# Performance work log

Hardware: AMD Instinct MI355X
Metric: run time of the kernel (lower is better)

The kernel has to match this reference:

```python
import jax, jax.numpy as jnp
import numpy as np

DIM = 512
HEADS = 8
DIM_HEAD = 64
LANDMARKS = 256
PINV_ITERS = 6
RES_K = 33


def layernorm(x, g, b, eps=1e-5):
    mu = jnp.mean(x, -1, keepdims=True)
    var = jnp.mean((x - mu) ** 2, -1, keepdims=True)
    return (x - mu) / jnp.sqrt(var + eps) * g + b


def moore_penrose_pinv(x, iters=PINV_ITERS):
    abs_x = jnp.abs(x)
    col = abs_x.sum(-1)
    row = abs_x.sum(-2)
    z = jnp.swapaxes(x, -1, -2) / (jnp.max(col) * jnp.max(row))
    I = jnp.eye(x.shape[-1], dtype=x.dtype)
    for _ in range(iters):
        xz = x @ z
        z = 0.25 * z @ (13.0 * I - xz @ (15.0 * I - xz @ (7.0 * I - xz)))
    return z


def nystrom_attention(x, Wqkv, Wout, bout, res_w):
    b, n, _ = x.shape
    m = LANDMARKS
    pad = (m - n % m) % m
    if pad:
        x = jnp.pad(x, ((0, 0), (pad, 0), (0, 0)))  # front pad, as in lucidrains impl
    qkv = x @ Wqkv  # (b, np, 3*inner)
    q, k, v = jnp.split(qkv, 3, axis=-1)
    to_heads = lambda t: t.reshape(b, -1, HEADS, DIM_HEAD).transpose(0, 2, 1, 3)
    q, k, v = to_heads(q), to_heads(k), to_heads(v)  # (b,h,np,d)
    q = q * (DIM_HEAD ** -0.5)
    l = -(-n // m)  # ceil(n/m), tokens per landmark
    ql = q.reshape(b, HEADS, m, l, DIM_HEAD).sum(3) / l  # (b,h,m,d)
    kl = k.reshape(b, HEADS, m, l, DIM_HEAD).sum(3) / l
    sim1 = jnp.einsum('bhid,bhjd->bhij', q, kl)   # (b,h,np,m)
    sim2 = jnp.einsum('bhid,bhjd->bhij', ql, kl)  # (b,h,m,m)
    sim3 = jnp.einsum('bhid,bhjd->bhij', ql, k)   # (b,h,m,np)
    a1 = jax.nn.softmax(sim1, -1)
    a2 = jax.nn.softmax(sim2, -1)
    a3 = jax.nn.softmax(sim3, -1)
    a2_inv = moore_penrose_pinv(a2)
    out = (a1 @ a2_inv) @ (a3 @ v)  # (b,h,np,d)
    # depthwise residual conv along sequence (kernel 33x1, groups=heads, no bias)
    res = jax.lax.conv_general_dilated(
        v, res_w, (1, 1), [(RES_K // 2, RES_K // 2), (0, 0)],
        dimension_numbers=('NCHW', 'OIHW', 'NCHW'), feature_group_count=HEADS)
    out = out + res
    out = out.transpose(0, 2, 1, 3).reshape(b, -1, HEADS * DIM_HEAD)
    out = out @ Wout + bout
    return out[:, -n:]


def depthwise2d(x, w, b, pad):
    y = jax.lax.conv_general_dilated(
        x, w, (1, 1), [(pad, pad), (pad, pad)],
        dimension_numbers=('NCHW', 'OIHW', 'NCHW'), feature_group_count=DIM)
    return y + b[None, :, None, None]


def ppeg(x, H, W, w7, b7, w5, b5, w3, b3):
    B, _, C = x.shape
    cls_tok, feat = x[:, :1], x[:, 1:]
    cnn = feat.transpose(0, 2, 1).reshape(B, C, H, W)
    y = depthwise2d(cnn, w7, b7, 3) + cnn + depthwise2d(cnn, w5, b5, 2) + depthwise2d(cnn, w3, b3, 1)
    y = y.reshape(B, C, H * W).transpose(0, 2, 1)
    return jnp.concatenate([cls_tok, y], axis=1)


def setup_inputs() -> dict:
    key = jax.random.key(0)
    ks = jax.random.split(key, 20)
    s = 0.02
    n_classes = 5
    inp = {
        'data': jax.random.normal(ks[0], (1, 15000, 1024), jnp.float32),
        'W_fc1': jax.random.normal(ks[1], (1024, DIM), jnp.float32) * s,
        'b_fc1': jnp.zeros((DIM,), jnp.float32),
        'cls_token': jax.random.normal(ks[2], (1, 1, DIM), jnp.float32),
        'ln1_g': jnp.ones((DIM,), jnp.float32), 'ln1_b': jnp.zeros((DIM,), jnp.float32),
        'qkv1': jax.random.normal(ks[3], (DIM, 3 * HEADS * DIM_HEAD), jnp.float32) * s,
        'out1_w': jax.random.normal(ks[4], (HEADS * DIM_HEAD, DIM), jnp.float32) * s,
        'out1_b': jnp.zeros((DIM,), jnp.float32),
        'res1': jax.random.normal(ks[5], (HEADS, 1, RES_K, 1), jnp.float32) * s,
        'w7': jax.random.normal(ks[6], (DIM, 1, 7, 7), jnp.float32) * s,
        'b7': jnp.zeros((DIM,), jnp.float32),
        'w5': jax.random.normal(ks[7], (DIM, 1, 5, 5), jnp.float32) * s,
        'b5': jnp.zeros((DIM,), jnp.float32),
        'w3': jax.random.normal(ks[8], (DIM, 1, 3, 3), jnp.float32) * s,
        'b3': jnp.zeros((DIM,), jnp.float32),
        'ln2_g': jnp.ones((DIM,), jnp.float32), 'ln2_b': jnp.zeros((DIM,), jnp.float32),
        'qkv2': jax.random.normal(ks[9], (DIM, 3 * HEADS * DIM_HEAD), jnp.float32) * s,
        'out2_w': jax.random.normal(ks[10], (HEADS * DIM_HEAD, DIM), jnp.float32) * s,
        'out2_b': jnp.zeros((DIM,), jnp.float32),
        'res2': jax.random.normal(ks[11], (HEADS, 1, RES_K, 1), jnp.float32) * s,
        'norm_g': jnp.ones((DIM,), jnp.float32), 'norm_b': jnp.zeros((DIM,), jnp.float32),
        'W_fc2': jax.random.normal(ks[12], (DIM, n_classes), jnp.float32) * s,
        'b_fc2': jnp.zeros((n_classes,), jnp.float32),
    }
    return inp


def reference(data, W_fc1, b_fc1, cls_token, ln1_g, ln1_b, qkv1, out1_w, out1_b, res1,
              w7, b7, w5, b5, w3, b3, ln2_g, ln2_b, qkv2, out2_w, out2_b, res2,
              norm_g, norm_b, W_fc2, b_fc2):
    h = jax.nn.relu(data @ W_fc1 + b_fc1)  # (B, N, 512)
    N = h.shape[1]
    _H = int(np.ceil(np.sqrt(N)))
    _W = _H
    add = _H * _W - N
    h = jnp.concatenate([h, h[:, :add]], axis=1)  # pad to square grid
    B = h.shape[0]
    h = jnp.concatenate([jnp.broadcast_to(cls_token, (B, 1, DIM)), h], axis=1)
    h = h + nystrom_attention(layernorm(h, ln1_g, ln1_b), qkv1, out1_w, out1_b, res1)
    h = ppeg(h, _H, _W, w7, b7, w5, b5, w3, b3)
    h = h + nystrom_attention(layernorm(h, ln2_g, ln2_b), qkv2, out2_w, out2_b, res2)
    h = layernorm(h, norm_g, norm_b)[:, 0]
    logits = h @ W_fc2 + b_fc2
    Y_prob = jax.nn.softmax(logits, -1)
    Y_hat = jnp.argmax(logits, -1)
    return logits, Y_prob, Y_hat
```

## Files before the change

### kernel.cpp

```cpp
#include <hip/hip_runtime.h>
#include <math.h>

#define NP 15360
#define NPQ 15488
#define NTOK 15130
#define HG 123

typedef __attribute__((ext_vector_type(8))) short s8b;
typedef __attribute__((ext_vector_type(4))) float f4;

__device__ inline float bf2f(ushort u) { return __uint_as_float(((unsigned)u) << 16); }
__device__ inline ushort f2bf(float f) {
    unsigned u = __float_as_uint(f);
    unsigned r = (u + 0x7fffu + ((u >> 16) & 1u)) >> 16;
    return (ushort)r;
}

__global__ __launch_bounds__(256)
void gemm_f32(const float* __restrict__ A, int lda, long sA,
              const float* __restrict__ B, int ldb, long sB,
              float* __restrict__ C, int ldc, long sC,
              int M, int N, int K,
              const float* __restrict__ bias,
              const float* __restrict__ E, int ldE, long sE, float eS,
              float cS, int relu, int accum)
{
    A += (long)blockIdx.z * sA;
    B += (long)blockIdx.z * sB;
    C += (long)blockIdx.z * sC;
    if (E) E += (long)blockIdx.z * sE;
    const int m0 = blockIdx.y * 64, n0 = blockIdx.x * 64;
    const int t = threadIdx.x;
    const int tx = t & 15, ty = t >> 4;
    __shared__ float As[16][64];
    __shared__ float Bs[16][64];
    float acc[4][4] = {};
    const int arow = t >> 2, akc = (t & 3) * 4;
    const int brow = t >> 4, bnc = (t & 15) * 4;
    for (int k0 = 0; k0 < K; k0 += 16) {
        float4 av = make_float4(0.f, 0.f, 0.f, 0.f);
        if (m0 + arow < M) av = *(const float4*)(A + (long)(m0 + arow) * lda + k0 + akc);
        As[akc + 0][arow] = av.x; As[akc + 1][arow] = av.y;
        As[akc + 2][arow] = av.z; As[akc + 3][arow] = av.w;
        float4 bv = *(const float4*)(B + (long)(k0 + brow) * ldb + n0 + bnc);
        *(float4*)&Bs[brow][bnc] = bv;
        __syncthreads();
#pragma unroll
        for (int kk = 0; kk < 16; ++kk) {
            float4 a4 = *(const float4*)&As[kk][ty * 4];
            float4 b4 = *(const float4*)&Bs[kk][tx * 4];
            float a[4] = {a4.x, a4.y, a4.z, a4.w};
            float b[4] = {b4.x, b4.y, b4.z, b4.w};
#pragma unroll
            for (int i = 0; i < 4; i++)
#pragma unroll
                for (int j = 0; j < 4; j++) acc[i][j] = fmaf(a[i], b[j], acc[i][j]);
        }
        __syncthreads();
    }
#pragma unroll
    for (int i = 0; i < 4; i++) {
        int m = m0 + ty * 4 + i;
        if (m < M) {
#pragma unroll
            for (int j = 0; j < 4; j++) {
                int n = n0 + tx * 4 + j;
                float v = cS * acc[i][j];
                if (E) v = fmaf(eS, E[(long)m * ldE + n], v);
                if (bias) v += bias[n];
                if (relu) v = fmaxf(v, 0.f);
                if (accum) C[(long)m * ldc + n] += v;
                else C[(long)m * ldc + n] = v;
            }
        }
    }
}

template<int MT, int NT, int WROWS, int WCOLS>
__global__ __launch_bounds__(256)
void gemm_mfma(const ushort* __restrict__ A, int lda, long sA,
               const ushort* __restrict__ Bt, int ldb, long sB,
               float* __restrict__ C, int ldc, long sC,
               int M, int K,
               const float* __restrict__ bias, int relu, int accum)
{
    constexpr int TM = MT * 16 * WROWS;
    constexpr int TN = NT * 16 * WCOLS;
    constexpr int BKP = 40;
    constexpr int AIT = TM / 64;
    constexpr int BIT = TN / 64;
    __shared__ ushort As[TM * BKP];
    __shared__ ushort Bs[TN * BKP];
    A  += (long)blockIdx.z * sA;
    Bt += (long)blockIdx.z * sB;
    C  += (long)blockIdx.z * sC;
    const int t = threadIdx.x;
    const int nwg = gridDim.x * gridDim.y;
    const int flat = blockIdx.y * gridDim.x + blockIdx.x;
    const int q8 = nwg >> 3, r8 = nwg & 7;
    const int xcd = flat & 7, idx = flat >> 3;
    const int swz = (xcd < r8) ? (xcd * (q8 + 1) + idx)
                               : (r8 * (q8 + 1) + (xcd - r8) * q8 + idx);
    const int m0 = (swz / gridDim.x) * TM;
    const int n0 = (swz % gridDim.x) * TN;
    const int w = t >> 6, l = t & 63;
    const int wm = (w / WCOLS) * (MT * 16), wn = (w % WCOLS) * (NT * 16);
    const int lr = l & 15;
    const int lk = (l >> 4) * 8;
    const int srow = t >> 2, skc = (t & 3) * 8;
    f4 acc[MT][NT] = {};
    s8b pa[AIT], pb[BIT];
#pragma unroll
    for (int i = 0; i < AIT; i++)
        pa[i] = *(const s8b*)(A + (long)(m0 + srow + i * 64) * lda + skc);
#pragma unroll
    for (int i = 0; i < BIT; i++)
        pb[i] = *(const s8b*)(Bt + (long)(n0 + srow + i * 64) * ldb + skc);
    for (int k0 = 0; k0 < K; k0 += 32) {
        __syncthreads();
#pragma unroll
        for (int i = 0; i < AIT; i++)
            *(s8b*)(&As[(srow + i * 64) * BKP + skc]) = pa[i];
#pragma unroll
        for (int i = 0; i < BIT; i++)
            *(s8b*)(&Bs[(srow + i * 64) * BKP + skc]) = pb[i];
        if (k0 + 32 < K) {
#pragma unroll
            for (int i = 0; i < AIT; i++)
                pa[i] = *(const s8b*)(A + (long)(m0 + srow + i * 64) * lda + k0 + 32 + skc);
#pragma unroll
            for (int i = 0; i < BIT; i++)
                pb[i] = *(const s8b*)(Bt + (long)(n0 + srow + i * 64) * ldb + k0 + 32 + skc);
        }
        __syncthreads();
        s8b af[MT], bf[NT];
#pragma unroll
        for (int i = 0; i < MT; i++) af[i] = *(const s8b*)(&As[(wm + i * 16 + lr) * BKP + lk]);
#pragma unroll
        for (int j = 0; j < NT; j++) bf[j] = *(const s8b*)(&Bs[(wn + j * 16 + lr) * BKP + lk]);
#pragma unroll
        for (int i = 0; i < MT; i++)
#pragma unroll
            for (int j = 0; j < NT; j++)
                acc[i][j] = __builtin_amdgcn_mfma_f32_16x16x32_bf16(af[i], bf[j], acc[i][j], 0, 0, 0);
    }
    const int orow = (l >> 4) * 4;
#pragma unroll
    for (int i = 0; i < MT; i++) {
#pragma unroll
        for (int r = 0; r < 4; r++) {
            int m = m0 + wm + i * 16 + orow + r;
            if (m < M) {
#pragma unroll
                for (int j = 0; j < NT; j++) {
                    int n = n0 + wn + j * 16 + lr;
                    float vv = acc[i][j][r];
                    if (bias) vv += bias[n];
                    if (relu) vv = fmaxf(vv, 0.f);
                    if (accum) C[(long)m * ldc + n] += vv;
                    else C[(long)m * ldc + n] = vv;
                }
            }
        }
    }
}

__global__ __launch_bounds__(256)
void gemm_nn16(const ushort* __restrict__ A, const ushort* __restrict__ B,
               const ushort* __restrict__ E, ushort* __restrict__ C,
               int N, int K, float cS, float eS, long sAB)
{
    __shared__ ushort As[64 * 40];
    __shared__ ushort Bs[64 * 40];
    A += (long)blockIdx.z * sAB;
    B += (long)blockIdx.z * sAB;
    if (E) E += (long)blockIdx.z * sAB;
    C += (long)blockIdx.z * sAB;
    const int t = threadIdx.x;
    const int m0 = blockIdx.y * 64, n0 = blockIdx.x * 64;
    const int w = t >> 6, l = t & 63;
    const int wm = (w >> 1) * 32, wn = (w & 1) * 32;
    const int lr = l & 15, lk = (l >> 4) * 8;
    f4 acc[2][2] = {};
    for (int k0 = 0; k0 < K; k0 += 32) {
        {
            int row = t >> 2, kc = (t & 3) * 8;
            s8b v = *(const s8b*)(A + (long)(m0 + row) * K + k0 + kc);
            *(s8b*)(&As[row * 40 + kc]) = v;
            int kk = t >> 3, nc = (t & 7) * 8;
            s8b vb = *(const s8b*)(B + (long)(k0 + kk) * N + n0 + nc);
#pragma unroll
            for (int j = 0; j < 8; j++) Bs[(nc + j) * 40 + kk] = ((ushort*)&vb)[j];
        }
        __syncthreads();
        s8b af[2], bf[2];
#pragma unroll
        for (int i = 0; i < 2; i++) af[i] = *(const s8b*)(&As[(wm + i * 16 + lr) * 40 + lk]);
#pragma unroll
        for (int j = 0; j < 2; j++) bf[j] = *(const s8b*)(&Bs[(wn + j * 16 + lr) * 40 + lk]);
#pragma unroll
        for (int i = 0; i < 2; i++)
#pragma unroll
            for (int j = 0; j < 2; j++)
                acc[i][j] = __builtin_amdgcn_mfma_f32_16x16x32_bf16(af[i], bf[j], acc[i][j], 0, 0, 0);
        __syncthreads();
    }
    const int orow = (l >> 4) * 4;
#pragma unroll
    for (int i = 0; i < 2; i++)
#pragma unroll
        for (int r = 0; r < 4; r++) {
            int m = m0 + wm + i * 16 + orow + r;
#pragma unroll
            for (int j = 0; j < 2; j++) {
                int n = n0 + wn + j * 16 + lr;
                float vv = cS * acc[i][j][r];
                if (E) vv = fmaf(eS, bf2f(E[(long)m * N + n]), vv);
                C[(long)m * N + n] = f2bf(vv);
            }
        }
}

__global__ __launch_bounds__(256)
void gemm_qkv_mfma(const ushort* __restrict__ A, const ushort* __restrict__ Bt,
                   ushort* __restrict__ qo, ushort* __restrict__ ko, ushort* __restrict__ vo)
{
    constexpr int BKP = 40;
    __shared__ ushort As[128 * BKP];
    __shared__ ushort Bs[128 * BKP];
    const int t = threadIdx.x;
    const int m0 = blockIdx.y * 128, n0 = blockIdx.x * 128;
    const int w = t >> 6, l = t & 63;
    const int wm = (w >> 1) * 64, wn = (w & 1) * 64;
    const int lr = l & 15;
    const int lk = (l >> 4) * 8;
    f4 acc[4][4] = {};
    for (int k0 = 0; k0 < 512; k0 += 32) {
        for (int c = t; c < 512; c += 256) {
            int row = c >> 2, kc = (c & 3) * 8;
            s8b va = *(const s8b*)(A + (long)(m0 + row) * 512 + k0 + kc);
            *(s8b*)(&As[row * BKP + kc]) = va;
            s8b vb = *(const s8b*)(Bt + (long)(n0 + row) * 512 + k0 + kc);
            *(s8b*)(&Bs[row * BKP + kc]) = vb;
        }
        __syncthreads();
        s8b af[4], bf[4];
#pragma unroll
        for (int i = 0; i < 4; i++) af[i] = *(const s8b*)(&As[(wm + i * 16 + lr) * BKP + lk]);
#pragma unroll
        for (int j = 0; j < 4; j++) bf[j] = *(const s8b*)(&Bs[(wn + j * 16 + lr) * BKP + lk]);
#pragma unroll
        for (int i = 0; i < 4; i++)
#pragma unroll
            for (int j = 0; j < 4; j++)
                acc[i][j] = __builtin_amdgcn_mfma_f32_16x16x32_bf16(af[i], bf[j], acc[i][j], 0, 0, 0);
        __syncthreads();
    }
    const int orow = (l >> 4) * 4;
#pragma unroll
    for (int i = 0; i < 4; i++) {
#pragma unroll
        for (int r = 0; r < 4; r++) {
            int m = m0 + wm + i * 16 + orow + r;
#pragma unroll
            for (int j = 0; j < 4; j++) {
                int col = n0 + wn + j * 16 + lr;
                int which = col >> 9, h = (col >> 6) & 7, d = col & 63;
                float vv = acc[i][j][r];
                if (which == 0) vv *= 0.125f;
                ushort* dst = which == 0 ? qo : (which == 1 ? ko : vo);
                dst[((long)h * NPQ + m) * 64 + d] = f2bf(vv);
            }
        }
    }
}

__global__ __launch_bounds__(256, 3)
void k_flash_a3v(const ushort* __restrict__ qlb, const ushort* __restrict__ kg,
                 const ushort* __restrict__ vg,
                 float* __restrict__ pacc, float* __restrict__ pml)
{
    const int c = blockIdx.x;
    const int qt = blockIdx.y;
    const int h = blockIdx.z;
    const int t = threadIdx.x;
    const int w = t >> 6, lane = t & 63;
    const int quad = lane >> 4, l16 = lane & 15;
    const s8b vones = {0x3F80, 0x3F80, 0x3F80, 0x3F80, 0x3F80, 0x3F80, 0x3F80, 0x3F80};

    __shared__ union {
        struct { ushort Vt[64][40]; ushort Ps[128][40]; } s;
        float Os[128][68];
    } L;

    s8b aq[2][2];
    const ushort* qbase = qlb + ((long)h * 256 + qt * 128 + w * 32) * 64;
#pragma unroll
    for (int mi = 0; mi < 2; mi++)
#pragma unroll
        for (int kf = 0; kf < 2; kf++)
            aq[mi][kf] = *(const s8b*)(qbase + (mi * 16 + l16) * 64 + kf * 32 + quad * 8);

    f4 oacc[2][4] = {};
    f4 lacc[2] = {};

    const ushort* kh = kg + (long)h * NPQ * 64;
    const ushort* vh = vg + (long)h * NPQ * 64;
    const int key0c = c * 256;

    const int vkk = (t >> 3) & 31;
    const int vdc = (t & 7) * 8;
    const int vcolp = (vkk + ((vdc >> 3) & 3) * 8) & 31;

    s8b vvN = *(const s8b*)(vh + (long)(key0c + vkk) * 64 + vdc);
    s8b bqN[2][2];
#pragma unroll
    for (int nj = 0; nj < 2; nj++)
#pragma unroll
        for (int kf = 0; kf < 2; kf++)
            bqN[nj][kf] = *(const s8b*)(kh + (long)(key0c + nj * 16 + l16) * 64 + kf * 32 + quad * 8);

#pragma unroll
    for (int sub = 0; sub < 8; sub++) {
        int key0 = key0c + sub * 32;
        s8b vvC = vvN;
        s8b bq[2][2];
#pragma unroll
        for (int nj = 0; nj < 2; nj++)
#pragma unroll
            for (int kf = 0; kf < 2; kf++) bq[nj][kf] = bqN[nj][kf];
        if (sub < 7) {
            vvN = *(const s8b*)(vh + (long)(key0 + 32 + vkk) * 64 + vdc);
#pragma unroll
            for (int nj = 0; nj < 2; nj++)
#pragma unroll
                for (int kf = 0; kf < 2; kf++)
                    bqN[nj][kf] = *(const s8b*)(kh + (long)(key0 + 32 + nj * 16 + l16) * 64 + kf * 32 + quad * 8);
        }
        __syncthreads();
        {
#pragma unroll
            for (int j = 0; j < 8; j++) L.s.Vt[vdc + j][vcolp] = ((ushort*)&vvC)[j];
        }
        f4 sacc[2][2] = {};
#pragma unroll
        for (int mi = 0; mi < 2; mi++)
#pragma unroll
            for (int nj = 0; nj < 2; nj++) {
                sacc[mi][nj] = __builtin_amdgcn_mfma_f32_16x16x32_bf16(aq[mi][0], bq[nj][0], sacc[mi][nj], 0, 0, 0);
                sacc[mi][nj] = __builtin_amdgcn_mfma_f32_16x16x32_bf16(aq[mi][1], bq[nj][1], sacc[mi][nj], 0, 0, 0);
            }
#pragma unroll
        for (int mi = 0; mi < 2; mi++)
#pragma unroll
            for (int r = 0; r < 4; r++) {
                int row = w * 32 + mi * 16 + quad * 4 + r;
                L.s.Ps[row][l16]      = f2bf(__expf(sacc[mi][0][r]));
                L.s.Ps[row][16 + l16] = f2bf(__expf(sacc[mi][1][r]));
            }
        __syncthreads();
        s8b ap[2], bv[4];
#pragma unroll
        for (int mi = 0; mi < 2; mi++)
            ap[mi] = *(const s8b*)(&L.s.Ps[w * 32 + mi * 16 + l16][quad * 8]);
#pragma unroll
        for (int dj = 0; dj < 4; dj++) {
            int d = dj * 16 + l16;
            int rot = (d >> 3) & 3;
            int cb = ((quad + rot) & 3) * 8;
            bv[dj] = *(const s8b*)(&L.s.Vt[d][cb]);
        }
#pragma unroll
        for (int mi = 0; mi < 2; mi++) {
#pragma unroll
            for (int dj = 0; dj < 4; dj++)
                oacc[mi][dj] = __builtin_amdgcn_mfma_f32_16x16x32_bf16(ap[mi], bv[dj], oacc[mi][dj], 0, 0, 0);
            lacc[mi] = __builtin_amdgcn_mfma_f32_16x16x32_bf16(ap[mi], vones, lacc[mi], 0, 0, 0);
        }
    }
    __syncthreads();
#pragma unroll
    for (int mi = 0; mi < 2; mi++)
#pragma unroll
        for (int dj = 0; dj < 4; dj++)
#pragma unroll
            for (int r = 0; r < 4; r++)
                L.Os[w * 32 + mi * 16 + quad * 4 + r][dj * 16 + l16] = oacc[mi][dj][r];
    long pbase = (long)(h * 60 + c);
    if (l16 == 0) {
#pragma unroll
        for (int mi = 0; mi < 2; mi++)
#pragma unroll
            for (int r = 0; r < 4; r++) {
                int i = qt * 128 + w * 32 + mi * 16 + quad * 4 + r;
                pml[pbase * 512 + i] = 0.f;
                pml[pbase * 512 + 256 + i] = lacc[mi][r];
            }
    }
    __syncthreads();
    float* pc = pacc + pbase * 16384 + qt * 128;
    int d = t >> 2, ig = t & 3;
#pragma unroll
    for (int u = 0; u < 8; u++) {
        int i0 = ig * 32 + u * 4;
        float4 v4 = make_float4(L.Os[i0][d], L.Os[i0 + 1][d], L.Os[i0 + 2][d], L.Os[i0 + 3][d]);
        *(float4*)(pc + (long)d * 256 + i0) = v4;
    }
}

__global__ __launch_bounds__(256, 3)
void k_attn1(const ushort* __restrict__ qg, const ushort* __restrict__ klb,
             const ushort* __restrict__ BmT, const ushort* __restrict__ vg,
             const float* __restrict__ rw, ushort* __restrict__ ohb)
{
    const int m0 = blockIdx.x * 128;
    const int h = blockIdx.y;
    const int t = threadIdx.x;
    const int w = t >> 6, lane = t & 63;
    const int quad = lane >> 4, l16 = lane & 15;
    const s8b vones = {0x3F80, 0x3F80, 0x3F80, 0x3F80, 0x3F80, 0x3F80, 0x3F80, 0x3F80};

    __shared__ union {
        ushort Ps[2][128][40];
        ushort Os[128][68];
    } L;
    __shared__ __attribute__((aligned(16))) ushort Vs[160][64];

    const ushort* vh = vg + (long)h * NPQ * 64;
    {
        const ushort* srcw = vh + (long)(214 + m0 + w * 40) * 64 + lane * 8;
        ushort* dstw = &Vs[w * 40][0];
#pragma unroll
        for (int it = 0; it < 5; it++)
            __builtin_amdgcn_global_load_lds(
                (const __attribute__((address_space(1))) void*)(srcw + it * 512),
                (__attribute__((address_space(3))) void*)(dstw + it * 512),
                16, 0, 0);
    }

    s8b aq[2][2];
    const ushort* qbase = qg + ((long)h * NPQ + 230 + m0 + w * 32) * 64;
#pragma unroll
    for (int mi = 0; mi < 2; mi++)
#pragma unroll
        for (int kf = 0; kf < 2; kf++)
            aq[mi][kf] = *(const s8b*)(qbase + (mi * 16 + l16) * 64 + kf * 32 + quad * 8);

    const ushort* kh = klb + (long)h * 16384;
    const ushort* bmt = BmT + (long)h * 16384;

    s8b bqN[2][2];
#pragma unroll
    for (int nj = 0; nj < 2; nj++)
#pragma unroll
        for (int kf = 0; kf < 2; kf++)
            bqN[nj][kf] = *(const s8b*)(kh + (long)(nj * 16 + l16) * 64 + kf * 32 + quad * 8);

    f4 oacc[2][4] = {};
    f4 lacc[2] = {};
#pragma unroll
    for (int sub = 0; sub < 8; sub++) {
        int key0 = sub * 32;
        s8b bq[2][2];
#pragma unroll
        for (int nj = 0; nj < 2; nj++)
#pragma unroll
            for (int kf = 0; kf < 2; kf++) bq[nj][kf] = bqN[nj][kf];
        if (sub < 7) {
#pragma unroll
            for (int nj = 0; nj < 2; nj++)
#pragma unroll
                for (int kf = 0; kf < 2; kf++)
                    bqN[nj][kf] = *(const s8b*)(kh + (long)(key0 + 32 + nj * 16 + l16) * 64 + kf * 32 + quad * 8);
        }
        s8b bv[4];
#pragma unroll
        for (int dj = 0; dj < 4; dj++)
            bv[dj] = *(const s8b*)(bmt + (long)(dj * 16 + l16) * 256 + key0 + quad * 8);
        f4 sacc[2][2] = {};
#pragma unroll
        for (int mi = 0; mi < 2; mi++)
#pragma unroll
            for (int nj = 0; nj < 2; nj++) {
                sacc[mi][nj] = __builtin_amdgcn_mfma_f32_16x16x32_bf16(aq[mi][0], bq[nj][0], sacc[mi][nj], 0, 0, 0);
                sacc[mi][nj] = __builtin_amdgcn_mfma_f32_16x16x32_bf16(aq[mi][1], bq[nj][1], sacc[mi][nj], 0, 0, 0);
            }
        int par = sub & 1;
#pragma unroll
        for (int mi = 0; mi < 2; mi++)
#pragma unroll
            for (int r = 0; r < 4; r++) {
                int row = w * 32 + mi * 16 + quad * 4 + r;
                L.Ps[par][row][l16]      = f2bf(__expf(sacc[mi][0][r]));
                L.Ps[par][row][16 + l16] = f2bf(__expf(sacc[mi][1][r]));
            }
        s8b ap[2];
#pragma unroll
        for (int mi = 0; mi < 2; mi++)
            ap[mi] = *(const s8b*)(&L.Ps[par][w * 32 + mi * 16 + l16][quad * 8]);
#pragma unroll
        for (int mi = 0; mi < 2; mi++) {
#pragma unroll
            for (int dj = 0; dj < 4; dj++)
                oacc[mi][dj] = __builtin_amdgcn_mfma_f32_16x16x32_bf16(ap[mi], bv[dj], oacc[mi][dj], 0, 0, 0);
            lacc[mi] = __builtin_amdgcn_mfma_f32_16x16x32_bf16(ap[mi], vones, lacc[mi], 0, 0, 0);
        }
    }
    __syncthreads();

    if (214 + m0 + 160 > NP) {
        for (int r = w * 32; r < w * 32 + 64 && r < 160; ++r)
            if (214 + m0 + r >= NP) Vs[r][lane] = 0;
    }

#pragma unroll
    for (int mi = 0; mi < 2; mi++)
#pragma unroll
        for (int r = 0; r < 4; r++) {
            float inv = 1.f / lacc[mi][r];
            int row = w * 32 + mi * 16 + quad * 4 + r;
#pragma unroll
            for (int dj = 0; dj < 4; dj++)
                L.Os[row][dj * 16 + l16] = f2bf(oacc[mi][dj][r] * inv);
        }
    float rwf[33];
#pragma unroll
    for (int kk = 0; kk < 33; kk++) rwf[kk] = rw[h * 33 + kk];
#pragma unroll
    for (int half = 0; half < 2; half++) {
        const int rbase = w * 32 + half * 16;
        float vr[48];
#pragma unroll
        for (int s = 0; s < 48; s++) vr[s] = bf2f(Vs[rbase + s][lane]);
        float conv[16];
#pragma unroll
        for (int i = 0; i < 16; i++) conv[i] = 0.f;
#pragma unroll
        for (int kk = 0; kk < 33; kk++) {
            float wk = rwf[kk];
#pragma unroll
            for (int i = 0; i < 16; i++) conv[i] = fmaf(wk, vr[i + kk], conv[i]);
        }
        int t0 = m0 + rbase;
#pragma unroll
        for (int i = 0; i < 16; i++) {
            int tk = t0 + i;
            if (tk < NTOK) {
                float val = bf2f(L.Os[rbase + i][lane]) + conv[i];
                ohb[(long)tk * 512 + h * 64 + lane] = f2bf(val);
            }
        }
    }
}

__global__ __launch_bounds__(256)
void k_layernorm(const float* __restrict__ h, ushort* __restrict__ xln,
                 const float* __restrict__ g, const float* __restrict__ b, int pad)
{
    int row = blockIdx.x, t = threadIdx.x;
    if (row < pad) {
        xln[(long)row * 512 + t] = 0;
        xln[(long)row * 512 + t + 256] = 0;
        return;
    }
    const float* src = h + (long)(row - pad) * 512;
    float x1 = src[t], x2 = src[t + 256];
    float s = x1 + x2, q = x1 * x1 + x2 * x2;
    __shared__ float rs[4], rq[4], st[2];
    int wid = t >> 6, lane = t & 63;
#pragma unroll
    for (int o = 32; o > 0; o >>= 1) { s += __shfl_down(s, o); q += __shfl_down(q, o); }
    if (lane == 0) { rs[wid] = s; rq[wid] = q; }
    __syncthreads();
    if (t == 0) {
        float S = rs[0] + rs[1] + rs[2] + rs[3];
        float Q = rq[0] + rq[1] + rq[2] + rq[3];
        float mean = S / 512.f;
        float var = Q / 512.f - mean * mean;
        st[0] = mean; st[1] = rsqrtf(var + 1e-5f);
    }
    __syncthreads();
    float mean = st[0], rstd = st[1];
    xln[(long)row * 512 + t] = f2bf((x1 - mean) * rstd * g[t] + b[t]);
    xln[(long)row * 512 + t + 256] = f2bf((x2 - mean) * rstd * g[t + 256] + b[t + 256]);
}

__global__ __launch_bounds__(256)
void k_padcls(float* __restrict__ hbuf, const float* __restrict__ cls)
{
    int i = blockIdx.x, t = threadIdx.x;
    if (i == 0) { hbuf[t] = cls[t]; hbuf[t + 256] = cls[t + 256]; }
    else {
        hbuf[(long)(15000 + i) * 512 + t] = hbuf[(long)i * 512 + t];
        hbuf[(long)(15000 + i) * 512 + t + 256] = hbuf[(long)i * 512 + t + 256];
    }
}

__global__ __launch_bounds__(256)
void k_wT(const float* __restrict__ Wm, ushort* __restrict__ Wt, int K, int N, long sW, long sWt)
{
    Wm += (long)blockIdx.z * sW; Wt += (long)blockIdx.z * sWt;
    __shared__ float tile[32][33];
    int tx = threadIdx.x & 31, ty = threadIdx.x >> 5;
    int n0 = blockIdx.x * 32, k0 = blockIdx.y * 32;
#pragma unroll
    for (int u = 0; u < 4; u++) tile[ty + u * 8][tx] = Wm[(long)(k0 + ty + u * 8) * N + n0 + tx];
    __syncthreads();
#pragma unroll
    for (int u = 0; u < 4; u++) Wt[(long)(n0 + ty + u * 8) * K + k0 + tx] = f2bf(tile[tx][ty + u * 8]);
}

__global__ __launch_bounds__(256)
void k_cvt(const float4* __restrict__ src, ushort4* __restrict__ dst, long n4)
{
    long i = (long)blockIdx.x * 256 + threadIdx.x;
    if (i < n4) {
        float4 v = src[i];
        ushort4 o;
        o.x = f2bf(v.x); o.y = f2bf(v.y); o.z = f2bf(v.z); o.w = f2bf(v.w);
        dst[i] = o;
    }
}

__global__ __launch_bounds__(256)
void k_b2f(const ushort4* __restrict__ src, float4* __restrict__ dst, long n4)
{
    long i = (long)blockIdx.x * 256 + threadIdx.x;
    if (i < n4) {
        ushort4 v = src[i];
        dst[i] = make_float4(bf2f(v.x), bf2f(v.y), bf2f(v.z), bf2f(v.w));
    }
}

__global__ __launch_bounds__(64)
void k_landmarks(const ushort* __restrict__ q, const ushort* __restrict__ k,
                 float* __restrict__ ql, ushort* __restrict__ qlb,
                 float* __restrict__ klT, ushort* __restrict__ klb,
                 unsigned* __restrict__ scal)
{
    int i = blockIdx.x, h = blockIdx.y, d = threadIdx.x;
    if (i == 0 && h == 0 && d == 0) { scal[0] = 0u; scal[1] = 0u; }
    long base = ((long)h * NPQ + (long)i * 60) * 64 + d;
    float sq = 0.f, sk = 0.f;
    for (int j = 0; j < 60; j++) { sq += bf2f(q[base + j * 64]); sk += bf2f(k[base + j * 64]); }
    float qv = sq / 60.f, kv = sk / 60.f;
    ql[((long)h * 256 + i) * 64 + d] = qv;
    qlb[((long)h * 256 + i) * 64 + d] = f2bf(qv);
    klT[((long)h * 64 + d) * 256 + i] = kv;
    klb[((long)h * 256 + i) * 64 + d] = f2bf(kv);
}

__global__ __launch_bounds__(256)
void k_softmax256(float* __restrict__ X, ushort* __restrict__ X16, long headStride)
{
    float* row = X + (long)blockIdx.y * headStride + (long)blockIdx.x * 256;
    int t = threadIdx.x, wid = t >> 6, lane = t & 63;
    float x = row[t];
    __shared__ float rm[4], rsum[4], fin[2];
    float m = x;
#pragma unroll
    for (int o = 32; o > 0; o >>= 1) m = fmaxf(m, __shfl_down(m, o));
    if (lane == 0) rm[wid] = m;
    __syncthreads();
    if (t == 0) fin[0] = fmaxf(fmaxf(rm[0], rm[1]), fmaxf(rm[2], rm[3]));
    __syncthreads();
    float e = __expf(x - fin[0]);
    float s = e;
#pragma unroll
    for (int o = 32; o > 0; o >>= 1) s += __shfl_down(s, o);
    if (lane == 0) rsum[wid] = s;
    __syncthreads();
    if (t == 0) fin[1] = rsum[0] + rsum[1] + rsum[2] + rsum[3];
    __syncthreads();
    float v = e / fin[1];
    row[t] = v;
    if (X16) X16[(long)blockIdx.y * headStride + (long)blockIdx.x * 256 + t] = f2bf(v);
}

__global__ __launch_bounds__(256)
void k_colmax(const float* __restrict__ a2, unsigned* __restrict__ scal)
{
    int h = blockIdx.x, t = threadIdx.x, wid = t >> 6, lane = t & 63;
    const float* A = a2 + (long)h * 65536;
    float cs = 0.f, rs = 0.f;
    for (int i = 0; i < 256; i++) cs += A[(long)i * 256 + t];
    for (int j = 0; j < 256; j++) rs += A[(long)t * 256 + j];
    __shared__ float r1[4], r2[4];
    float m1v = cs, m2v = rs;
#pragma unroll
    for (int o = 32; o > 0; o >>= 1) {
        m1v = fmaxf(m1v, __shfl_down(m1v, o));
        m2v = fmaxf(m2v, __shfl_down(m2v, o));
    }
    if (lane == 0) { r1[wid] = m1v; r2[wid] = m2v; }
    __syncthreads();
    if (t == 0) {
        float a = fmaxf(fmaxf(r1[0], r1[1]), fmaxf(r1[2], r1[3]));
        float b = fmaxf(fmaxf(r2[0], r2[1]), fmaxf(r2[2], r2[3]));
        atomicMax(scal + 0, __float_as_uint(a));
        atomicMax(scal + 1, __float_as_uint(b));
    }
}

__global__ __launch_bounds__(256)
void k_zinit(const float* __restrict__ a2, ushort* __restrict__ zb, const unsigned* __restrict__ scal)
{
    float s = 1.f / (__uint_as_float(scal[0]) * __uint_as_float(scal[1]));
    const float* A = a2 + (long)blockIdx.z * 65536;
    ushort* Z = zb + (long)blockIdx.z * 65536;
    __shared__ float tile[32][33];
    int tx = threadIdx.x & 31, ty = threadIdx.x >> 5;
    int i0 = blockIdx.x * 32, j0 = blockIdx.y * 32;
#pragma unroll
    for (int u = 0; u < 4; u++) tile[ty + u * 8][tx] = A[(long)(j0 + ty + u * 8) * 256 + i0 + tx];
    __syncthreads();
#pragma unroll
    for (int u = 0; u < 4; u++) Z[(long)(i0 + ty + u * 8) * 256 + j0 + tx] = f2bf(tile[tx][ty + u * 8] * s);
}

__global__ __launch_bounds__(256)
void k_a3v_merge(const float* __restrict__ pacc, const float* __restrict__ pml,
                 float* __restrict__ t1)
{
    int d = blockIdx.x, h = blockIdx.y, i = threadIdx.x;
    float M = -INFINITY, L = 0.f, num = 0.f;
    for (int c = 0; c < 60; c++) {
        float mc = pml[(long)(h * 60 + c) * 2 * 256 + i];
        float lc = pml[((long)(h * 60 + c) * 2 + 1) * 256 + i];
        float ac = pacc[((long)(h * 60 + c) * 64 + d) * 256 + i];
        if (mc > M) {
            float f = __expf(M - mc);
            num = num * f + ac; L = L * f + lc; M = mc;
        } else {
            float p = __expf(mc - M);
            num = fmaf(p, ac, num); L = fmaf(p, lc, L);
        }
    }
    t1[((long)h * 256 + i) * 64 + d] = num / L;
}

__global__ __launch_bounds__(256)
void k_cls(const ushort* __restrict__ qb, const float* __restrict__ klT,
           const float* __restrict__ Bm, const ushort* __restrict__ vb,
           const float* __restrict__ rw, float* __restrict__ oh)
{
    int h = blockIdx.x, t = threadIdx.x, wid = t >> 6, lane = t & 63;
    __shared__ float qs[64], p[256], red[256];
    __shared__ float rm[4], rsum[4], fin[2];
    if (t < 64) qs[t] = bf2f(qb[((long)h * NPQ + 230) * 64 + t]);
    __syncthreads();
    float s = 0.f;
    for (int d = 0; d < 64; d++) s = fmaf(qs[d], klT[((long)h * 64 + d) * 256 + t], s);
    float m = s;
#pragma unroll
    for (int o = 32; o > 0; o >>= 1) m = fmaxf(m, __shfl_down(m, o));
    if (lane == 0) rm[wid] = m;
    __syncthreads();
    if (t == 0) fin[0] = fmaxf(fmaxf(rm[0], rm[1]), fmaxf(rm[2], rm[3]));
    __syncthreads();
    float e = __expf(s - fin[0]);
    float ss = e;
#pragma unroll
    for (int o = 32; o > 0; o >>= 1) ss += __shfl_down(ss, o);
    if (lane == 0) rsum[wid] = ss;
    __syncthreads();
    if (t == 0) fin[1] = rsum[0] + rsum[1] + rsum[2] + rsum[3];
    __syncthreads();
    p[t] = e / fin[1];
    __syncthreads();
    int d = t & 63, grp = t >> 6;
    float o = 0.f;
    for (int j = grp * 64; j < grp * 64 + 64; j++) o = fmaf(p[j], Bm[((long)h * 256 + j) * 64 + d], o);
    red[t] = o;
    __syncthreads();
    if (t < 64) {
        float val = red[t] + red[t + 64] + red[t + 128] + red[t + 192];
#pragma unroll
        for (int kk = 0; kk < 33; kk++)
            val = fmaf(rw[h * 33 + kk], bf2f(vb[((long)h * NPQ + 214 + kk) * 64 + t]), val);
        oh[h * 64 + t] = val;
    }
}

__global__ __launch_bounds__(256)
void k_copy4(const float4* __restrict__ src, float4* __restrict__ dst, long n4)
{
    long i = (long)blockIdx.x * 256 + threadIdx.x;
    if (i < n4) dst[i] = src[i];
}

__global__ __launch_bounds__(512)
void k_wcomb(const float* __restrict__ w7, const float* __restrict__ b7,
             const float* __restrict__ w5, const float* __restrict__ b5,
             const float* __restrict__ w3, const float* __restrict__ b3,
             float* __restrict__ wc, float* __restrict__ bc)
{
    int k = blockIdx.x, c = threadIdx.x;
    int kr = k / 7, kc = k % 7;
    float v = w7[c * 49 + k];
    if (kr >= 1 && kr <= 5 && kc >= 1 && kc <= 5) v += w5[c * 25 + (kr - 1) * 5 + (kc - 1)];
    if (kr >= 2 && kr <= 4 && kc >= 2 && kc <= 4) v += w3[c * 9 + (kr - 2) * 3 + (kc - 2)];
    if (k == 24) v += 1.f;
    wc[k * 512 + c] = v;
    if (k == 0) bc[c] = b7[c] + b5[c] + b3[c];
}

__global__ __launch_bounds__(256, 4)
void k_ppeg4(const float* __restrict__ cnn, float* __restrict__ hbuf,
             const float* __restrict__ wc, const float* __restrict__ bc)
{
    __shared__ __attribute__((aligned(16))) float tile[320 * 32];
    const int t = threadIdx.x;
    const int w = t >> 6, lane = t & 63;
    const int c0 = blockIdx.x * 16;
    const int r0 = blockIdx.y * 8;
    const int cb = blockIdx.z * 32;
    {
        const int pl = lane >> 3;
        const int c4 = (lane & 7) * 4;
#pragma unroll
        for (int it = 0; it < 10; ++it) {
            int chunk = w * 10 + it;
            int pos = chunk * 8 + pl;
            int pr = pos / 22, pc = pos - pr * 22;
            int gr = r0 + pr - 3, gc = c0 + pc - 3;
            int grc = min(max(gr, 0), HG - 1), gcc = min(max(gc, 0), HG - 1);
            const float* src = cnn + (long)(grc * HG + gcc) * 512 + cb + c4;
            __builtin_amdgcn_global_load_lds(
                (const __attribute__((address_space(1))) void*)src,
                (__attribute__((address_space(3))) void*)(tile + chunk * 256),
                16, 0, 0);
        }
    }
    __syncthreads();
    const bool boundary = (r0 < 3) | (r0 > HG - 11) | (c0 < 3) | (c0 > HG - 19);
    if (boundary) {
        for (int pos = t; pos < 308; pos += 256) {
            int pr = pos / 22, pc = pos - pr * 22;
            int gr = r0 + pr - 3, gc = c0 + pc - 3;
            if (gr < 0 || gr >= HG || gc < 0 || gc >= HG) {
                float4 z = make_float4(0.f, 0.f, 0.f, 0.f);
#pragma unroll
                for (int c4 = 0; c4 < 32; c4 += 4) *(float4*)&tile[pos * 32 + c4] = z;
            }
        }
        __syncthreads();
    }
    const int cp = t & 15;
    const int slot = t >> 4;
    const int orow = slot >> 1;
    const int ohalf = (slot & 1) * 8;
    float a0[8], a1[8];
#pragma unroll
    for (int i = 0; i < 8; i++) { a0[i] = 0.f; a1[i] = 0.f; }
    for (int kr = 0; kr < 7; kr++) {
        float w0[14], w1[14];
        const float* trow = tile + ((orow + kr) * 22 + ohalf) * 32 + cp * 2;
#pragma unroll
        for (int j = 0; j < 14; j++) {
            float2 v = *(const float2*)(trow + j * 32);
            w0[j] = v.x; w1[j] = v.y;
        }
#pragma unroll
        for (int kc = 0; kc < 7; kc++) {
            float2 wv = *(const float2*)(wc + (long)(kr * 7 + kc) * 512 + cb + cp * 2);
#pragma unroll
            for (int i = 0; i < 8; i++) {
                a0[i] = fmaf(wv.x, w0[i + kc], a0[i]);
                a1[i] = fmaf(wv.y, w1[i + kc], a1[i]);
            }
        }
    }
    const float2 bv = *(const float2*)(bc + cb + cp * 2);
    const int gr = r0 + orow;
    if (gr < HG) {
#pragma unroll
        for (int i = 0; i < 8; i++) {
            int gc = c0 + ohalf + i;
            if (gc < HG) {
                float* dst = hbuf + (long)(1 + gr * HG + gc) * 512 + cb + cp * 2;
                dst[0] = a0[i] + bv.x;
                dst[1] = a1[i] + bv.y;
            }
        }
    }
}

__global__ __launch_bounds__(256)
void k_final(const float* __restrict__ hbuf, const float* __restrict__ g,
             const float* __restrict__ b, const float* __restrict__ W2,
             const float* __restrict__ b2, float* __restrict__ out)
{
    __shared__ float y[512];
    __shared__ float rs[4], rq[4], st[2], lg[8];
    int t = threadIdx.x, wid = t >> 6, lane = t & 63;
    float x1 = hbuf[t], x2 = hbuf[t + 256];
    float s = x1 + x2, q = x1 * x1 + x2 * x2;
#pragma unroll
    for (int o = 32; o > 0; o >>= 1) { s += __shfl_down(s, o); q += __shfl_down(q, o); }
    if (lane == 0) { rs[wid] = s; rq[wid] = q; }
    __syncthreads();
    if (t == 0) {
        float S = rs[0] + rs[1] + rs[2] + rs[3];
        float Q = rq[0] + rq[1] + rq[2] + rq[3];
        float mean = S / 512.f;
        float var = Q / 512.f - mean * mean;
        st[0] = mean; st[1] = rsqrtf(var + 1e-5f);
    }
    __syncthreads();
    float mean = st[0], rstd = st[1];
    y[t] = (x1 - mean) * rstd * g[t] + b[t];
    y[t + 256] = (x2 - mean) * rstd * g[t + 256] + b[t + 256];
    __syncthreads();
    if (t < 5) {
        float acc = b2[t];
        for (int kx = 0; kx < 512; kx++) acc = fmaf(y[kx], W2[kx * 5 + t], acc);
        lg[t] = acc;
    }
    __syncthreads();
    if (t == 0) {
        float mx = lg[0]; int am = 0;
        for (int j = 1; j < 5; j++) if (lg[j] > mx) { mx = lg[j]; am = j; }
        float e[5], se = 0.f;
        for (int j = 0; j < 5; j++) { e[j] = __expf(lg[j] - mx); se += e[j]; }
        for (int j = 0; j < 5; j++) { out[j] = lg[j]; out[5 + j] = e[j] / se; }
        out[10] = (float)am;
    }
}

extern "C" void kernel_launch(void* const* d_in, const int* in_sizes, int n_in,
                              void* d_out, int out_size, void* d_ws, size_t ws_size,
                              hipStream_t stream)
{
    const float* data  = (const float*)d_in[0];
    const float* Wfc1  = (const float*)d_in[1];
    const float* bfc1  = (const float*)d_in[2];
    const float* cls   = (const float*)d_in[3];
    const float* ln1g  = (const float*)d_in[4];
    const float* ln1b  = (const float*)d_in[5];
    const float* qkv1  = (const float*)d_in[6];
    const float* out1w = (const float*)d_in[7];
    const float* out1b = (const float*)d_in[8];
    const float* res1  = (const float*)d_in[9];
    const float* w7    = (const float*)d_in[10];
    const float* b7    = (const float*)d_in[11];
    const float* w5    = (const float*)d_in[12];
    const float* b5    = (const float*)d_in[13];
    const float* w3    = (const float*)d_in[14];
    const float* b3    = (const float*)d_in[15];
    const float* ln2g  = (const float*)d_in[16];
    const float* ln2b  = (const float*)d_in[17];
    const float* qkv2  = (const float*)d_in[18];
    const float* out2w = (const float*)d_in[19];
    const float* out2b = (const float*)d_in[20];
    const float* res2  = (const float*)d_in[21];
    const float* normg = (const float*)d_in[22];
    const float* normb = (const float*)d_in[23];
    const float* Wfc2  = (const float*)d_in[24];
    const float* bfc2  = (const float*)d_in[25];
    float* out = (float*)d_out;

    float* W = (float*)d_ws;
    size_t off = 0;
    auto alloc = [&](size_t n) { size_t o = off; off += (n + 255) & ~(size_t)255; return o; };
    float*  hbuf   = W + alloc((size_t)NTOK * 512);
    float*  ohreg  = W + alloc((size_t)15232 * 512);
    float*  oh     = ohreg;
    ushort* xln    = (ushort*)ohreg;
    ushort* qb16   = (ushort*)(W + alloc((size_t)8 * NPQ * 32));
    ushort* kb16   = (ushort*)(W + alloc((size_t)8 * NPQ * 32));
    ushort* vb16   = (ushort*)(W + alloc((size_t)8 * NPQ * 32));
    float*  ql     = W + alloc(8 * 256 * 64);
    ushort* qlb    = (ushort*)(W + alloc(8 * 256 * 32));
    float*  klT    = W + alloc(8 * 64 * 256);
    ushort* klb    = (ushort*)(W + alloc(8 * 256 * 32));
    float*  a2     = W + alloc(8 * 65536);
    ushort* a2b    = (ushort*)(W + alloc(8 * 32768));
    ushort* zb0    = (ushort*)(W + alloc(8 * 32768));
    ushort* zb1    = (ushort*)(W + alloc(8 * 32768));
    ushort* m1b    = (ushort*)(W + alloc(8 * 32768));
    ushort* mab    = (ushort*)(W + alloc(8 * 32768));
    ushort* mbb    = (ushort*)(W + alloc(8 * 32768));
    float*  z0     = W + alloc(8 * 65536);
    float*  t1     = W + alloc(8 * 256 * 64);
    float*  Bm     = W + alloc(8 * 256 * 64);
    ushort* BmbT   = (ushort*)(W + alloc(8 * 256 * 32));
    float*  scal   = W + alloc(64);
    ushort* ohb16  = (ushort*)(W + alloc((size_t)15232 * 256));
    ushort* WfcT   = (ushort*)(W + alloc(1024 * 256));
    ushort* qkv1T  = (ushort*)(W + alloc(1536 * 256));
    ushort* qkv2T  = (ushort*)(W + alloc(1536 * 256));
    ushort* out1T  = (ushort*)(W + alloc(512 * 256));
    ushort* out2T  = (ushort*)(W + alloc(512 * 256));
    float*  wc     = W + alloc(49 * 512);
    float*  bc     = W + alloc(512);
    float*  big    = W + alloc(8110080);
    ushort* datab  = (ushort*)big;
    float*  pacc   = big;
    float*  pml    = big + 7864320;
    float*  cnn    = big;
    if (ws_size < off * sizeof(float)) return;

    k_wT<<<dim3(16, 32, 1), 256, 0, stream>>>(Wfc1, WfcT, 1024, 512, 0, 0);
    k_wT<<<dim3(48, 16, 1), 256, 0, stream>>>(qkv1, qkv1T, 512, 1536, 0, 0);
    k_wT<<<dim3(48, 16, 1), 256, 0, stream>>>(qkv2, qkv2T, 512, 1536, 0, 0);
    k_wT<<<dim3(16, 16, 1), 256, 0, stream>>>(out1w, out1T, 512, 512, 0, 0);
    k_wT<<<dim3(16, 16, 1), 256, 0, stream>>>(out2w, out2T, 512, 512, 0, 0);
    k_wcomb<<<49, 512, 0, stream>>>(w7, b7, w5, b5, w3, b3, wc, bc);
    k_cvt<<<15000, 256, 0, stream>>>((const float4*)data, (ushort4*)datab, 3840000);
    gemm_mfma<2, 4, 2, 2><<<dim3(4, 235, 1), 256, 0, stream>>>(
        datab, 1024, 0, WfcT, 1024, 0, hbuf + 512, 512, 0, 15000, 1024, bfc1, 1, 0);
    k_padcls<<<130, 256, 0, stream>>>(hbuf, cls);

    auto layer = [&](const float* lng, const float* lnb, const ushort* qkvT,
                     const float* outW, const ushort* outT, const float* outB,
                     const float* resW, bool full) {
        k_layernorm<<<NP, 256, 0, stream>>>(hbuf, xln, lng, lnb, 230);
        gemm_qkv_mfma<<<dim3(12, 120, 1), 256, 0, stream>>>(xln, qkvT, qb16, kb16, vb16);
        k_landmarks<<<dim3(256, 8), 64, 0, stream>>>(qb16, kb16, ql, qlb, klT, klb, (unsigned*)scal);
        gemm_f32<<<dim3(4, 4, 8), 256, 0, stream>>>(ql, 64, 16384, klT, 256, 16384,
            a2, 256, 65536, 256, 256, 64, nullptr, nullptr, 0, 0, 0.f, 1.f, 0, 0);
        k_softmax256<<<dim3(256, 8), 256, 0, stream>>>(a2, a2b, 65536);
        k_colmax<<<8, 256, 0, stream>>>(a2, (unsigned*)scal);
        k_zinit<<<dim3(8, 8, 8), 256, 0, stream>>>(a2, zb0, (const unsigned*)scal);
        ushort* zbi = zb0; ushort* zbo = zb1;
        for (int it = 0; it < 6; ++it) {
            gemm_nn16<<<dim3(4, 4, 8), 256, 0, stream>>>(a2b, zbi, nullptr, m1b, 256, 256, 1.f, 0.f, 65536);
            gemm_nn16<<<dim3(4, 4, 8), 256, 0, stream>>>(m1b, m1b, m1b, mab, 256, 256, -1.f, 7.f, 65536);
            gemm_nn16<<<dim3(4, 4, 8), 256, 0, stream>>>(m1b, mab, m1b, mbb, 256, 256, -1.f, 15.f, 65536);
            gemm_nn16<<<dim3(4, 4, 8), 256, 0, stream>>>(zbi, mbb, zbi, zbo, 256, 256, -0.25f, 3.25f, 65536);
            ushort* tmp = zbi; zbi = zbo; zbo = tmp;
        }
        k_b2f<<<512, 256, 0, stream>>>((const ushort4*)zbi, (float4*)z0, 131072);
        k_flash_a3v<<<dim3(60, 2, 8), 256, 0, stream>>>(qlb, kb16, vb16, pacc, pml);
        k_a3v_merge<<<dim3(64, 8), 256, 0, stream>>>(pacc, pml, t1);
        gemm_f32<<<dim3(1, 4, 8), 256, 0, stream>>>(z0, 256, 65536, t1, 64, 16384,
            Bm, 64, 16384, 256, 64, 256, nullptr, nullptr, 0, 0, 0.f, 1.f, 0, 0);
        if (full) {
            k_wT<<<dim3(2, 8, 8), 256, 0, stream>>>(Bm, BmbT, 256, 64, 16384, 16384);
            k_attn1<<<dim3(119, 8), 256, 0, stream>>>(qb16, klb, BmbT, vb16, resW, ohb16);
            gemm_mfma<2, 4, 2, 2><<<dim3(4, 237, 1), 256, 0, stream>>>(
                ohb16, 512, 0, outT, 512, 0, hbuf, 512, 0, NTOK, 512, outB, 0, 1);
        } else {
            k_cls<<<8, 256, 0, stream>>>(qb16, klT, Bm, vb16, resW, oh);
            gemm_f32<<<dim3(8, 1, 1), 256, 0, stream>>>(oh, 512, 0, outW, 512, 0,
                hbuf, 512, 0, 1, 512, 512, outB, nullptr, 0, 0, 0.f, 1.f, 0, 1);
        }
    };

    layer(ln1g, ln1b, qkv1T, out1w, out1T, out1b, res1, true);
    k_copy4<<<(1936512 + 255) / 256, 256, 0, stream>>>((const float4*)(hbuf + 512), (float4*)cnn, 1936512);
    k_ppeg4<<<dim3(8, 16, 16), 256, 0, stream>>>(cnn, hbuf, wc, bc);
    layer(ln2g, ln2b, qkv2T, out2w, out2T, out2b, res2, false);
    k_final<<<1, 256, 0, stream>>>(hbuf, normg, normb, Wfc2, bfc2, out);
}
```

Before: 1.148 ms.

## Prefetch next K tile into registers and swizzle QKV GEMM blocks across XCDs

The QKV projection GEMM now loads the next K-slice of A and B into registers while the current slice is consumed by MFMAs. This overlaps global memory latency with compute and moves the barrier so each iteration still needs only two syncs. It also remaps block indices so consecutive tiles land on the same XCD, which is meant to improve L2 reuse. The cost is extra register pressure from the prefetch buffers.

```diff
diff --git a/kernel.cpp b/kernel.cpp
--- a/kernel.cpp
+++ b/kernel.cpp
@@ -229,19 +229,39 @@
     __shared__ ushort As[128 * BKP];
     __shared__ ushort Bs[128 * BKP];
     const int t = threadIdx.x;
-    const int m0 = blockIdx.y * 128, n0 = blockIdx.x * 128;
+    const int nwg = gridDim.x * gridDim.y;
+    const int flat = blockIdx.y * gridDim.x + blockIdx.x;
+    const int q8 = nwg >> 3, r8 = nwg & 7;
+    const int xcd = flat & 7, idx = flat >> 3;
+    const int swz = (xcd < r8) ? (xcd * (q8 + 1) + idx)
+                               : (r8 * (q8 + 1) + (xcd - r8) * q8 + idx);
+    const int m0 = (swz / gridDim.x) * 128;
+    const int n0 = (swz % gridDim.x) * 128;
     const int w = t >> 6, l = t & 63;
     const int wm = (w >> 1) * 64, wn = (w & 1) * 64;
     const int lr = l & 15;
     const int lk = (l >> 4) * 8;
+    const int srow = t >> 2, skc = (t & 3) * 8;
     f4 acc[4][4] = {};
+    s8b pa[2], pb[2];
+#pragma unroll
+    for (int i = 0; i < 2; i++) {
+        pa[i] = *(const s8b*)(A + (long)(m0 + srow + i * 64) * 512 + skc);
+        pb[i] = *(const s8b*)(Bt + (long)(n0 + srow + i * 64) * 512 + skc);
+    }
     for (int k0 = 0; k0 < 512; k0 += 32) {
-        for (int c = t; c < 512; c += 256) {
-            int row = c >> 2, kc = (c & 3) * 8;
-            s8b va = *(const s8b*)(A + (long)(m0 + row) * 512 + k0 + kc);
-            *(s8b*)(&As[row * BKP + kc]) = va;
-            s8b vb = *(const s8b*)(Bt + (long)(n0 + row) * 512 + k0 + kc);
-            *(s8b*)(&Bs[row * BKP + kc]) = vb;
+        __syncthreads();
+#pragma unroll
+        for (int i = 0; i < 2; i++) {
+            *(s8b*)(&As[(srow + i * 64) * BKP + skc]) = pa[i];
+            *(s8b*)(&Bs[(srow + i * 64) * BKP + skc]) = pb[i];
+        }
+        if (k0 + 32 < 512) {
+#pragma unroll
+            for (int i = 0; i < 2; i++) {
+                pa[i] = *(const s8b*)(A + (long)(m0 + srow + i * 64) * 512 + k0 + 32 + skc);
+                pb[i] = *(const s8b*)(Bt + (long)(n0 + srow + i * 64) * 512 + k0 + 32 + skc);
+            }
         }
         __syncthreads();
         s8b af[4], bf[4];
@@ -254,7 +274,6 @@
 #pragma unroll
             for (int j = 0; j < 4; j++)
                 acc[i][j] = __builtin_amdgcn_mfma_f32_16x16x32_bf16(af[i], bf[j], acc[i][j], 0, 0, 0);
-        __syncthreads();
     }
     const int orow = (l >> 4) * 4;
 #pragma unroll
```

Result: no change. 1.131 ms (-1.5%).
